# Kernel tuning notes

Measured on AMD Instinct MI355X. Metric: run time of the kernel, lower is better.

## Reference

```python
import jax, jax.numpy as jnp
import numpy as np
import math

IMG_SIZE = 768
NUM_CLASSES = 90
THRESHOLD = 0.05
IOU_THRESHOLD = 0.5
MAX_DETECTIONS = 100
K_CAND = 512  # per-class candidate pool before greedy NMS
RATIOS = [(1.0, 1.0), (1.4, 0.7), (0.7, 1.4)]
SCALES = [2 ** 0, 2 ** (1.0 / 3.0), 2 ** (2.0 / 3.0)]


def _generate_anchors():
    anchor_scale = 4.0
    pyramid_levels = [3, 4, 5, 6, 7]
    all_levels = []
    for lv in pyramid_levels:
        stride = 2 ** lv
        size = anchor_scale * 2 ** lv
        grid = IMG_SIZE // stride
        sx = np.arange(grid) * stride
        sy, sx = np.meshgrid(np.arange(grid) * stride, sx, indexing='ij')
        # torch meshgrid(shift_y, shift_x, indexing='ij') -> rows are y
        yy, xx = np.meshgrid(np.arange(grid) * stride, np.arange(grid) * stride, indexing='ij')
        shifts = np.stack([xx.ravel(), yy.ravel(), xx.ravel(), yy.ravel()], axis=1).astype(np.float32)
        base = []
        for r in RATIOS:
            for s in SCALES:
                w = size * s * math.sqrt(r[0] / r[1])
                h = size * s * math.sqrt(r[1] / r[0])
                base.append([-w / 2, -h / 2, w / 2, h / 2])
        base = np.asarray(base, dtype=np.float32)  # [9,4]
        anc = (base[None, :, :] + shifts[:, None, :]).reshape(-1, 4)
        all_levels.append(anc)
    return np.concatenate(all_levels, axis=0)  # [110484,4]


def setup_inputs() -> dict:
    key = jax.random.key(0)
    k1, k2, k3 = jax.random.split(key, 3)
    A = 110484
    x = jax.random.normal(k1, (1, 3, IMG_SIZE, IMG_SIZE), dtype=jnp.float32)
    regression = jax.random.normal(k2, (1, A, 4), dtype=jnp.float32) * 0.3
    classification = jax.random.normal(k3, (1, A, NUM_CLASSES), dtype=jnp.float32) - 2.0
    anchors = jnp.asarray(_generate_anchors())
    return {"x": x, "regression": regression, "classification": classification, "anchors": anchors}


def _decode_and_clip(anchors, deltas, H, W):
    # BBoxTransform (RetinaNet-style): deltas = (dx, dy, dw, dh)
    wa = anchors[:, 2] - anchors[:, 0]
    ha = anchors[:, 3] - anchors[:, 1]
    cxa = anchors[:, 0] + 0.5 * wa
    cya = anchors[:, 1] + 0.5 * ha
    dx, dy, dw, dh = deltas[:, 0], deltas[:, 1], deltas[:, 2], deltas[:, 3]
    cx = cxa + dx * wa
    cy = cya + dy * ha
    w = jnp.exp(dw) * wa
    h = jnp.exp(dh) * ha
    x1 = jnp.clip(cx - 0.5 * w, 0.0, W)
    y1 = jnp.clip(cy - 0.5 * h, 0.0, H)
    x2 = jnp.clip(cx + 0.5 * w, 0.0, W)
    y2 = jnp.clip(cy + 0.5 * h, 0.0, H)
    return jnp.stack([x1, y1, x2, y2], axis=1)  # [A,4]


def _pairwise_iou(b):  # [K,4] -> [K,K]
    area = (b[:, 2] - b[:, 0]) * (b[:, 3] - b[:, 1])
    xx1 = jnp.maximum(b[:, None, 0], b[None, :, 0])
    yy1 = jnp.maximum(b[:, None, 1], b[None, :, 1])
    xx2 = jnp.minimum(b[:, None, 2], b[None, :, 2])
    yy2 = jnp.minimum(b[:, None, 3], b[None, :, 3])
    inter = jnp.clip(xx2 - xx1, 0.0) * jnp.clip(yy2 - yy1, 0.0)
    return inter / (area[:, None] + area[None, :] - inter + 1e-8)


def _greedy_nms(iou_c, valid_c):
    # boxes are pre-sorted by descending score; fixed-iteration greedy NMS
    def step(suppressed, i):
        keep_i = valid_c[i] & jnp.logical_not(suppressed[i])
        suppressed = jnp.where(keep_i, suppressed | (iou_c[i] > IOU_THRESHOLD), suppressed)
        return suppressed, keep_i
    _, keep = jax.lax.scan(step, jnp.zeros(iou_c.shape[0], dtype=bool), jnp.arange(iou_c.shape[0]))
    return keep  # [K]


def _postprocess(x, regression, classification, anchors):
    H, W = x.shape[2], x.shape[3]
    boxes = _decode_and_clip(anchors, regression[0], float(H), float(W))  # [A,4]
    scores = jax.nn.sigmoid(classification[0])                            # [A,C]
    # per-class top-K candidate pool (sorted desc), fixed-shape NMS
    vals, idx = jax.lax.top_k(scores.T, K_CAND)        # [C,K]
    cand = boxes[idx]                                   # [C,K,4]
    valid = vals > THRESHOLD                            # [C,K]
    iou = jax.vmap(_pairwise_iou)(cand)                 # [C,K,K]
    keep = jax.vmap(_greedy_nms)(iou, valid)            # [C,K]
    kept_scores = jnp.where(keep, vals, -1.0).reshape(-1)  # [C*K]
    top_vals, flat_idx = jax.lax.top_k(kept_scores, MAX_DETECTIONS)
    labels = (flat_idx // K_CAND).astype(jnp.float32)
    det_boxes = cand.reshape(-1, 4)[flat_idx]
    ok = top_vals > 0.0
    det = jnp.concatenate([
        jnp.zeros((MAX_DETECTIONS, 1), dtype=jnp.float32),  # batch ids (batch=1 -> 0)
        det_boxes,
        top_vals[:, None],
        labels[:, None],
    ], axis=1)  # [100,7]
    return jnp.where(ok[:, None], det, 0.0)


def reference(x, regression, classification, anchors):
    return _postprocess(x, regression, classification, anchors)
```

## Files before the change

### kernel.cpp

```cpp
#include <hip/hip_runtime.h>
#include <math.h>


#define A_N   110484
#define C_N   90
#define KCAND 512
#define NBINS 8192
#define KSH   19
#define MAXDET 100
#define IMG_F 768.0f
#define THRESH 0.05f
#define VTOT  (A_N / 4)
#define SL_CAP 2048
#define KEEP_CAP 100
#define T_BLKS ((A_N + 63) / 64)
#define SEL_T 512
#define D_BLKS ((A_N + SEL_T - 1) / SEL_T)
#define FCAP  512

typedef unsigned int u32;
typedef unsigned long long u64;

__device__ __forceinline__ u32 fkey(float f) {
    u32 u = __float_as_uint(f);
    return (u & 0x80000000u) ? ~u : (u | 0x80000000u);
}
__device__ __forceinline__ float unfkey(u32 k) {
    u32 u = (k & 0x80000000u) ? (k ^ 0x80000000u) : ~k;
    return __uint_as_float(u);
}
__device__ __forceinline__ u64 shflx64(u64 v, int m) {
    u32 lo = (u32)__shfl_xor((int)(u32)v, m, 64);
    u32 hi = (u32)__shfl_xor((int)(v >> 32), m, 64);
    return ((u64)hi << 32) | lo;
}

__global__ __launch_bounds__(256)
void prep_kernel(const float* __restrict__ cls,
                 u32* __restrict__ keysT) {
    __shared__ u32 tile[64 * 91];
    const int a0 = blockIdx.x * 64;
    const int lim = min(64, A_N - a0);
    const int n4 = (lim * C_N) >> 2;
    const float4* src4 = (const float4*)(cls + (size_t)a0 * C_N);
    for (int i4 = threadIdx.x; i4 < n4; i4 += 256) {
        float4 x4 = src4[i4];
        const u32 base = (u32)(4 * i4);
        float xs[4] = { x4.x, x4.y, x4.z, x4.w };
        #pragma unroll
        for (int k = 0; k < 4; ++k) {
            u32 i = base + k;
            u32 aa = i / C_N, c = i % C_N;
            float s = 1.0f / (1.0f + expf(-xs[k]));
            tile[aa * 91 + c] = fkey(s);
        }
    }
    __syncthreads();
    for (int j = threadIdx.x; j < C_N * 64; j += 256) {
        int c = j >> 6, aa = j & 63;
        if (aa < lim)
            keysT[(size_t)c * A_N + a0 + aa] = tile[aa * 91 + c];
    }
}

__global__ __launch_bounds__(SEL_T)
void select_kernel(const u32* __restrict__ keysT,
                   const float* __restrict__ anchors,
                   const float* __restrict__ reg,
                   float4* __restrict__ boxes,
                   u64* __restrict__ candbuf) {
    __shared__ u32 hist[NBINS / 2];
    __shared__ u32 csum[SEL_T];
    __shared__ u64 lbuf[SL_CAP];
    __shared__ u32 sPv;
    __shared__ int lcnt;
    const int tid = threadIdx.x;

    if (blockIdx.x >= C_N) {
        int a = (blockIdx.x - C_N) * SEL_T + tid;
        if (a < A_N) {
            float4 an = ((const float4*)anchors)[a];
            float4 dl = ((const float4*)reg)[a];
            float wa = an.z - an.x, ha = an.w - an.y;
            float cx = an.x + 0.5f * wa + dl.x * wa;
            float cy = an.y + 0.5f * ha + dl.y * ha;
            float w = expf(dl.z) * wa;
            float h = expf(dl.w) * ha;
            float4 o;
            o.x = fminf(fmaxf(cx - 0.5f * w, 0.0f), IMG_F);
            o.y = fminf(fmaxf(cy - 0.5f * h, 0.0f), IMG_F);
            o.z = fminf(fmaxf(cx + 0.5f * w, 0.0f), IMG_F);
            o.w = fminf(fmaxf(cy + 0.5f * h, 0.0f), IMG_F);
            boxes[a] = o;
        }
        return;
    }
    const int c = blockIdx.x;
    const uint4* kv = (const uint4*)(keysT + (size_t)c * A_N);

    for (int i = tid; i < NBINS / 2; i += SEL_T) hist[i] = 0;
    if (tid == 0) { sPv = 0; lcnt = 0; }
    __syncthreads();

    #define HACC(K) do { \
        u32 b0 = (K).x >> KSH, b1 = (K).y >> KSH, b2 = (K).z >> KSH, b3 = (K).w >> KSH; \
        atomicAdd(&hist[b0 >> 1], 1u << ((b0 & 1) << 4)); \
        atomicAdd(&hist[b1 >> 1], 1u << ((b1 & 1) << 4)); \
        atomicAdd(&hist[b2 >> 1], 1u << ((b2 & 1) << 4)); \
        atomicAdd(&hist[b3 >> 1], 1u << ((b3 & 1) << 4)); } while (0)
    {
        int i = tid;
        for (; i + 3 * SEL_T < VTOT; i += 4 * SEL_T) {
            uint4 ka = kv[i], kb = kv[i + SEL_T], kc = kv[i + 2 * SEL_T], kd = kv[i + 3 * SEL_T];
            HACC(ka); HACC(kb); HACC(kc); HACC(kd);
        }
        for (; i < VTOT; i += SEL_T) { uint4 ka = kv[i]; HACC(ka); }
    }
    __syncthreads();

    u32 own = 0;
    {
        const int wb = (NBINS / 2) - 8 - 8 * tid;
        const int g = (tid >> 2) & 7;
        #pragma unroll
        for (int jj = 0; jj < 8; ++jj) {
            u32 v = hist[wb + ((g + jj) & 7)];
            own += (v & 0xffffu) + (v >> 16);
        }
    }
    csum[tid] = own;
    __syncthreads();
    for (int off = 1; off < SEL_T; off <<= 1) {
        u32 v = csum[tid];
        u32 a = (tid >= off) ? csum[tid - off] : 0u;
        __syncthreads();
        csum[tid] = v + a;
        __syncthreads();
    }
    const u32 incl = csum[tid], excl = incl - own;
    if (excl < (u32)KCAND && incl >= (u32)KCAND) {
        u32 cum = excl;
        const int hb = NBINS - 1 - 16 * tid;
        for (int j = 0; j < 16; ++j) {
            int b = hb - j;
            u32 v = hist[b >> 1];
            u32 cnt = (b & 1) ? (v >> 16) : (v & 0xffffu);
            if (cum + cnt >= (u32)KCAND) { sPv = (u32)b; break; }
            cum += cnt;
        }
    }
    __syncthreads();
    const u32 P = sPv;

    #define CACC(K, BASE) do { \
        if (((K).x >> KSH) >= P) { int p = atomicAdd(&lcnt, 1); if (p < SL_CAP) lbuf[p] = (((u64)(~(K).x)) << 32) | (u32)(BASE); } \
        if (((K).y >> KSH) >= P) { int p = atomicAdd(&lcnt, 1); if (p < SL_CAP) lbuf[p] = (((u64)(~(K).y)) << 32) | (u32)((BASE) + 1); } \
        if (((K).z >> KSH) >= P) { int p = atomicAdd(&lcnt, 1); if (p < SL_CAP) lbuf[p] = (((u64)(~(K).z)) << 32) | (u32)((BASE) + 2); } \
        if (((K).w >> KSH) >= P) { int p = atomicAdd(&lcnt, 1); if (p < SL_CAP) lbuf[p] = (((u64)(~(K).w)) << 32) | (u32)((BASE) + 3); } } while (0)
    {
        int i = tid;
        for (; i + 3 * SEL_T < VTOT; i += 4 * SEL_T) {
            uint4 ka = kv[i], kb = kv[i + SEL_T], kc = kv[i + 2 * SEL_T], kd = kv[i + 3 * SEL_T];
            CACC(ka, 4 * i); CACC(kb, 4 * (i + SEL_T)); CACC(kc, 4 * (i + 2 * SEL_T)); CACC(kd, 4 * (i + 3 * SEL_T));
        }
        for (; i < VTOT; i += SEL_T) { uint4 ka = kv[i]; CACC(ka, 4 * i); }
    }
    __syncthreads();
    const int n = min(lcnt, SL_CAP);
    for (int q = tid; q < SL_CAP; q += SEL_T) if (q >= n) lbuf[q] = ~0ULL;
    __syncthreads();

    {
        const int l = tid & 63, w = tid >> 6;
        int ii[4]; u64 v[4];
        #pragma unroll
        for (int r = 0; r < 4; ++r) { ii[r] = 256 * w + 64 * r + l; v[r] = lbuf[ii[r]]; }
        __syncthreads();
        #pragma unroll
        for (u32 kk = 2; kk <= (u32)SL_CAP; kk <<= 1) {
            #pragma unroll
            for (u32 j = kk >> 1; j > 0; j >>= 1) {
                if (j >= 256) {
                    #pragma unroll
                    for (int r = 0; r < 4; ++r) lbuf[ii[r]] = v[r];
                    __syncthreads();
                    #pragma unroll
                    for (int r = 0; r < 4; ++r) {
                        u64 pv = lbuf[ii[r] ^ j];
                        bool up = ((ii[r] & kk) == 0);
                        bool m = (((ii[r] & j) == 0) == up);
                        v[r] = m ? (v[r] < pv ? v[r] : pv) : (v[r] > pv ? v[r] : pv);
                    }
                    __syncthreads();
                } else if (j >= 64) {
                    const int rx = (int)(j >> 6);
                    u64 nv[4];
                    #pragma unroll
                    for (int r = 0; r < 4; ++r) {
                        u64 pv = v[r ^ rx];
                        bool up = ((ii[r] & kk) == 0);
                        bool m = (((ii[r] & j) == 0) == up);
                        nv[r] = m ? (v[r] < pv ? v[r] : pv) : (v[r] > pv ? v[r] : pv);
                    }
                    #pragma unroll
                    for (int r = 0; r < 4; ++r) v[r] = nv[r];
                } else {
                    #pragma unroll
                    for (int r = 0; r < 4; ++r) {
                        u64 pv = shflx64(v[r], (int)j);
                        bool up = ((ii[r] & kk) == 0);
                        bool m = (((ii[r] & j) == 0) == up);
                        v[r] = m ? (v[r] < pv ? v[r] : pv) : (v[r] > pv ? v[r] : pv);
                    }
                }
            }
        }
        u64* cb = candbuf + (size_t)c * KCAND;
        #pragma unroll
        for (int r = 0; r < 4; ++r)
            if (ii[r] < KCAND) cb[ii[r]] = v[r];
    }
}

__global__ __launch_bounds__(1024, 4)
void nms_kernel(const u64* __restrict__ candbuf,
                const float4* __restrict__ boxes,
                u32* __restrict__ keptbuf, u32* __restrict__ cnt2) {
    __shared__ u32 bmask[KCAND * 16];
    __shared__ float4 bb4[KCAND];
    __shared__ float sc[KCAND];
    __shared__ u32 keepf[16], wbase[17];
    const int c = blockIdx.x, tid = threadIdx.x;
    const int l = tid & 63, w = tid >> 6;

    if (tid < KCAND) {
        u64 e = candbuf[(size_t)c * KCAND + tid];
        sc[tid] = unfkey(~((u32)(e >> 32)));
        bb4[tid] = boxes[(u32)e];
    }
    if (tid < 16) keepf[tid] = 0;
    __syncthreads();

    {
        const float4 cj0 = bb4[0 * 64 + l], cj1 = bb4[1 * 64 + l];
        const float4 cj2 = bb4[2 * 64 + l], cj3 = bb4[3 * 64 + l];
        const float4 cj4 = bb4[4 * 64 + l], cj5 = bb4[5 * 64 + l];
        const float4 cj6 = bb4[6 * 64 + l], cj7 = bb4[7 * 64 + l];
        const float aj0 = (cj0.z - cj0.x) * (cj0.w - cj0.y);
        const float aj1 = (cj1.z - cj1.x) * (cj1.w - cj1.y);
        const float aj2 = (cj2.z - cj2.x) * (cj2.w - cj2.y);
        const float aj3 = (cj3.z - cj3.x) * (cj3.w - cj3.y);
        const float aj4 = (cj4.z - cj4.x) * (cj4.w - cj4.y);
        const float aj5 = (cj5.z - cj5.x) * (cj5.w - cj5.y);
        const float aj6 = (cj6.z - cj6.x) * (cj6.w - cj6.y);
        const float aj7 = (cj7.z - cj7.x) * (cj7.w - cj7.y);

        #define QSTEP(QQ, CJ, AJ) do { \
            if (QQ >= q0) { \
                float xx1 = fmaxf(bi.x, (CJ).x), yy1 = fmaxf(bi.y, (CJ).y); \
                float xx2 = fminf(bi.z, (CJ).z), yy2 = fminf(bi.w, (CJ).w); \
                float inter = fmaxf(xx2 - xx1, 0.0f) * fmaxf(yy2 - yy1, 0.0f); \
                float uni = ai + (AJ) - inter + 1e-8f; \
                bool sup = ((QQ * 64 + l) > r) && (inter > 0.5f * uni); \
                u64 bal = __ballot(sup); \
                if (l == 0) *(u64*)(row + 2 * QQ) = bal; \
            } } while (0)

        for (int r = w; r < KCAND; r += 16) {
            const float4 bi = bb4[r];
            const float ai = (bi.z - bi.x) * (bi.w - bi.y);
            const int q0 = (r + 1) >> 6;
            u32* row = bmask + r * 16;
            if (l < 2 * q0) row[l] = 0;
            QSTEP(0, cj0, aj0); QSTEP(1, cj1, aj1);
            QSTEP(2, cj2, aj2); QSTEP(3, cj3, aj3);
            QSTEP(4, cj4, aj4); QSTEP(5, cj5, aj5);
            QSTEP(6, cj6, aj6); QSTEP(7, cj7, aj7);
        }
        #undef QSTEP
    }
    __syncthreads();

    if (tid < 64) {
        const int lw = tid & 15;
        u32 removed = 0, keepw = 0;
        u32 rA[8], rB[8]; float sA[8], sB[8];
        #pragma unroll
        for (int k = 0; k < 8; ++k) { rA[k] = bmask[k * 16 + lw]; sA[k] = sc[k]; }
        #pragma unroll 1
        for (int ch = 0; ch < 64; ch += 2) {
            const int tb1 = (ch + 1) * 8;
            #pragma unroll
            for (int k = 0; k < 8; ++k) { rB[k] = bmask[(tb1 + k) * 16 + lw]; sB[k] = sc[tb1 + k]; }
            {
                const int tb = ch * 8;
                #pragma unroll
                for (int k = 0; k < 8; ++k) {
                    const int t = tb + k;
                    u32 rw = (u32)__builtin_amdgcn_readlane((int)removed, t >> 5);
                    bool d = (sA[k] > THRESH) && (((rw >> (t & 31)) & 1u) == 0u);
                    removed |= d ? rA[k] : 0u;
                    keepw |= (d && (tid == (t >> 5))) ? (1u << (t & 31)) : 0u;
                }
            }
            const int tb2 = (ch + 2 < 64) ? (ch + 2) * 8 : 0;
            #pragma unroll
            for (int k = 0; k < 8; ++k) { rA[k] = bmask[(tb2 + k) * 16 + lw]; sA[k] = sc[tb2 + k]; }
            {
                #pragma unroll
                for (int k = 0; k < 8; ++k) {
                    const int t = tb1 + k;
                    u32 rw = (u32)__builtin_amdgcn_readlane((int)removed, t >> 5);
                    bool d = (sB[k] > THRESH) && (((rw >> (t & 31)) & 1u) == 0u);
                    removed |= d ? rB[k] : 0u;
                    keepw |= (d && (tid == (t >> 5))) ? (1u << (t & 31)) : 0u;
                }
            }
            u32 cnt = (u32)__popc(keepw);
            #pragma unroll
            for (int m = 32; m; m >>= 1) cnt += (u32)__shfl_xor((int)cnt, m, 64);
            if (cnt >= (u32)KEEP_CAP) break;
        }
        if (tid < 16) keepf[tid] = keepw;
    }
    __syncthreads();

    if (tid == 0) {
        u32 t = 0;
        for (int q = 0; q < 16; ++q) { wbase[q] = t; t += __popc(keepf[q]); }
        wbase[16] = t;
        cnt2[c] = (t < (u32)KEEP_CAP) ? t : (u32)KEEP_CAP;
    }
    __syncthreads();
    if (tid < KCAND) {
        u32 word = keepf[tid >> 5];
        u32 bit = (u32)tid & 31u;
        if ((word >> bit) & 1u) {
            u32 rank = wbase[tid >> 5] + __popc(word & ((1u << bit) - 1u));
            if (rank < (u32)KEEP_CAP) {
                float s = sc[tid];
                float4 b = bb4[tid];
                uint4 a2, b2;
                a2.x = ~fkey(s);
                a2.y = (u32)(c * KCAND + tid);
                a2.z = __float_as_uint(b.x);
                a2.w = __float_as_uint(b.y);
                b2.x = __float_as_uint(b.z);
                b2.y = __float_as_uint(b.w);
                b2.z = __float_as_uint(s);
                b2.w = 0u;
                uint4* e = (uint4*)(keptbuf + ((size_t)c * KEEP_CAP + rank) * 8);
                e[0] = a2; e[1] = b2;
            }
        }
    }
}

__global__ __launch_bounds__(1024)
void final_kernel(const u32* __restrict__ keptbuf, const u32* __restrict__ cnt2,
                  float* __restrict__ out) {
    __shared__ u32 hist[NBINS];
    __shared__ u32 csum[1024];
    __shared__ u64 ebuf[FCAP];
    __shared__ u32 eidx[FCAP];
    __shared__ u32 scnt[C_N];
    __shared__ u32 sP;
    __shared__ int sN;
    const int tid = threadIdx.x;
    const int TOT = C_N * KEEP_CAP;

    for (int i = tid; i < MAXDET * 7; i += 1024) out[i] = 0.0f;
    for (int i = tid; i < NBINS; i += 1024) hist[i] = 0;
    if (tid < C_N) scnt[tid] = cnt2[tid];
    if (tid == 0) { sN = 0; sP = NBINS - 1; }
    __syncthreads();

    for (int i = tid; i < TOT; i += 1024) {
        u32 c = (u32)i / KEEP_CAP, pp = (u32)i % KEEP_CAP;
        if (pp < scnt[c]) {
            u32 khi = keptbuf[(size_t)i * 8];
            atomicAdd(&hist[khi >> KSH], 1u);
        }
    }
    __syncthreads();
    u32 own = 0; const int lo = 8 * tid;
    #pragma unroll
    for (int j = 0; j < 8; ++j) own += hist[lo + j];
    csum[tid] = own;
    __syncthreads();
    for (int off = 1; off < 1024; off <<= 1) {
        u32 v = csum[tid];
        u32 a = (tid >= off) ? csum[tid - off] : 0u;
        __syncthreads();
        csum[tid] = v + a;
        __syncthreads();
    }
    const u32 incl = csum[tid], excl = incl - own;
    if (excl < (u32)MAXDET && incl >= (u32)MAXDET) {
        u32 cum = excl;
        for (int j = 0; j < 8; ++j) {
            u32 h = hist[lo + j];
            if (cum + h >= (u32)MAXDET) { sP = (u32)(lo + j); break; }
            cum += h;
        }
    }
    __syncthreads();
    const u32 P = sP;
    for (int i = tid; i < TOT; i += 1024) {
        u32 c = (u32)i / KEEP_CAP, pp = (u32)i % KEEP_CAP;
        if (pp < scnt[c]) {
            const uint2 v2 = *((const uint2*)(keptbuf + (size_t)i * 8));
            if ((v2.x >> KSH) <= P) {
                int p = atomicAdd(&sN, 1);
                if (p < FCAP) {
                    ebuf[p] = ((u64)v2.x << 32) | v2.y;
                    eidx[p] = (u32)i;
                }
            }
        }
    }
    __syncthreads();
    const int n = min(sN, FCAP);
    u32 m = 128; while ((int)m < n) m <<= 1;
    for (int i = tid; i < (int)m; i += 1024) if (i >= n) ebuf[i] = ~0ULL;
    __syncthreads();
    for (u32 kk = 2; kk <= m; kk <<= 1) {
        for (u32 j = kk >> 1; j > 0; j >>= 1) {
            u32 i = (u32)tid;
            if (i < m) {
                u32 ixj = i ^ j;
                if (ixj > i) {
                    u64 x = ebuf[i], y = ebuf[ixj];
                    bool up = ((i & kk) == 0);
                    if (up ? (x > y) : (x < y)) {
                        ebuf[i] = y; ebuf[ixj] = x;
                        u32 t = eidx[i]; eidx[i] = eidx[ixj]; eidx[ixj] = t;
                    }
                }
            }
            __syncthreads();
        }
    }
    if (tid < MAXDET && tid < n) {
        u64 comp = ebuf[tid];
        if (comp != ~0ULL) {
            const uint4* e = (const uint4*)(keptbuf + (size_t)eidx[tid] * 8);
            uint4 a = e[0], b = e[1];
            float* o = out + tid * 7;
            o[0] = 0.0f;
            o[1] = __uint_as_float(a.z); o[2] = __uint_as_float(a.w);
            o[3] = __uint_as_float(b.x); o[4] = __uint_as_float(b.y);
            o[5] = __uint_as_float(b.z);
            o[6] = (float)(((u32)comp) >> 9);
        }
    }
}

extern "C" void kernel_launch(void* const* d_in, const int* in_sizes, int n_in,
                              void* d_out, int out_size, void* d_ws, size_t ws_size,
                              hipStream_t stream) {
    const float* reg     = (const float*)d_in[1];
    const float* cls     = (const float*)d_in[2];
    const float* anchors = (const float*)d_in[3];
    float* out = (float*)d_out;

    char* ws = (char*)d_ws;
    size_t off = 0;
    auto alloc = [&](size_t bytes) -> void* {
        void* p = ws + off;
        off = (off + bytes + 255) & ~(size_t)255;
        return p;
    };
    u32*    keysT   = (u32*)   alloc((size_t)C_N * A_N * sizeof(u32));
    float4* boxes   = (float4*)alloc((size_t)A_N * sizeof(float4));
    u64*    candbuf = (u64*)   alloc((size_t)C_N * KCAND * sizeof(u64));
    u32*    keptbuf = (u32*)   alloc((size_t)C_N * KEEP_CAP * 8 * sizeof(u32));
    u32*    cnt2    = (u32*)   alloc((size_t)C_N * sizeof(u32));
    (void)ws_size;

    prep_kernel<<<T_BLKS, 256, 0, stream>>>(cls, keysT);
    select_kernel<<<C_N + D_BLKS, SEL_T, 0, stream>>>(keysT, anchors, reg, boxes, candbuf);
    nms_kernel<<<C_N, 1024, 0, stream>>>(candbuf, boxes, keptbuf, cnt2);
    final_kernel<<<1, 1024, 0, stream>>>(keptbuf, cnt2, out);
}
```

Baseline: 204.0 us.

## Move box decoding into prep kernel and double select block size

Box decoding moves from extra blocks of the select kernel into extra blocks of the prep kernel, so the select kernel launches only the 90 per-class blocks. The select kernel now uses 1024 threads per block, with deeper 8-way unrolled key loads and a rebalanced histogram scan and bitonic sort that holds two elements per thread. The aim is more parallelism and memory-level parallelism per class, since only 90 blocks run on a GPU with many CUs. The trade-off is more register and LDS pressure per block and more block-wide barriers in the scan.

Result: faster. 190.1 us (-6.8%).

```diff
diff --git a/kernel.cpp b/kernel.cpp
--- a/kernel.cpp
+++ b/kernel.cpp
@@ -14,8 +14,8 @@
 #define SL_CAP 2048
 #define KEEP_CAP 100
 #define T_BLKS ((A_N + 63) / 64)
-#define SEL_T 512
-#define D_BLKS ((A_N + SEL_T - 1) / SEL_T)
+#define PD_BLKS ((A_N + 255) / 256)
+#define SEL_T 1024
 #define FCAP  512
 
 typedef unsigned int u32;
@@ -37,8 +37,30 @@
 
 __global__ __launch_bounds__(256)
 void prep_kernel(const float* __restrict__ cls,
-                 u32* __restrict__ keysT) {
+                 const float* __restrict__ anchors,
+                 const float* __restrict__ reg,
+                 u32* __restrict__ keysT,
+                 float4* __restrict__ boxes) {
     __shared__ u32 tile[64 * 91];
+    if (blockIdx.x >= T_BLKS) {
+        int a = (blockIdx.x - T_BLKS) * 256 + threadIdx.x;
+        if (a < A_N) {
+            float4 an = ((const float4*)anchors)[a];
+            float4 dl = ((const float4*)reg)[a];
+            float wa = an.z - an.x, ha = an.w - an.y;
+            float cx = an.x + 0.5f * wa + dl.x * wa;
+            float cy = an.y + 0.5f * ha + dl.y * ha;
+            float w = expf(dl.z) * wa;
+            float h = expf(dl.w) * ha;
+            float4 o;
+            o.x = fminf(fmaxf(cx - 0.5f * w, 0.0f), IMG_F);
+            o.y = fminf(fmaxf(cy - 0.5f * h, 0.0f), IMG_F);
+            o.z = fminf(fmaxf(cx + 0.5f * w, 0.0f), IMG_F);
+            o.w = fminf(fmaxf(cy + 0.5f * h, 0.0f), IMG_F);
+            boxes[a] = o;
+        }
+        return;
+    }
     const int a0 = blockIdx.x * 64;
     const int lim = min(64, A_N - a0);
     const int n4 = (lim * C_N) >> 2;
@@ -65,9 +87,6 @@
 
 __global__ __launch_bounds__(SEL_T)
 void select_kernel(const u32* __restrict__ keysT,
-                   const float* __restrict__ anchors,
-                   const float* __restrict__ reg,
-                   float4* __restrict__ boxes,
                    u64* __restrict__ candbuf) {
     __shared__ u32 hist[NBINS / 2];
     __shared__ u32 csum[SEL_T];
@@ -75,26 +94,6 @@
     __shared__ u32 sPv;
     __shared__ int lcnt;
     const int tid = threadIdx.x;
-
-    if (blockIdx.x >= C_N) {
-        int a = (blockIdx.x - C_N) * SEL_T + tid;
-        if (a < A_N) {
-            float4 an = ((const float4*)anchors)[a];
-            float4 dl = ((const float4*)reg)[a];
-            float wa = an.z - an.x, ha = an.w - an.y;
-            float cx = an.x + 0.5f * wa + dl.x * wa;
-            float cy = an.y + 0.5f * ha + dl.y * ha;
-            float w = expf(dl.z) * wa;
-            float h = expf(dl.w) * ha;
-            float4 o;
-            o.x = fminf(fmaxf(cx - 0.5f * w, 0.0f), IMG_F);
-            o.y = fminf(fmaxf(cy - 0.5f * h, 0.0f), IMG_F);
-            o.z = fminf(fmaxf(cx + 0.5f * w, 0.0f), IMG_F);
-            o.w = fminf(fmaxf(cy + 0.5f * h, 0.0f), IMG_F);
-            boxes[a] = o;
-        }
-        return;
-    }
     const int c = blockIdx.x;
     const uint4* kv = (const uint4*)(keysT + (size_t)c * A_N);
 
@@ -110,9 +109,11 @@
         atomicAdd(&hist[b3 >> 1], 1u << ((b3 & 1) << 4)); } while (0)
     {
         int i = tid;
-        for (; i + 3 * SEL_T < VTOT; i += 4 * SEL_T) {
-            uint4 ka = kv[i], kb = kv[i + SEL_T], kc = kv[i + 2 * SEL_T], kd = kv[i + 3 * SEL_T];
-            HACC(ka); HACC(kb); HACC(kc); HACC(kd);
+        for (; i + 7 * SEL_T < VTOT; i += 8 * SEL_T) {
+            uint4 k0 = kv[i], k1 = kv[i + SEL_T], k2 = kv[i + 2 * SEL_T], k3 = kv[i + 3 * SEL_T];
+            uint4 k4 = kv[i + 4 * SEL_T], k5 = kv[i + 5 * SEL_T], k6 = kv[i + 6 * SEL_T], k7 = kv[i + 7 * SEL_T];
+            HACC(k0); HACC(k1); HACC(k2); HACC(k3);
+            HACC(k4); HACC(k5); HACC(k6); HACC(k7);
         }
         for (; i < VTOT; i += SEL_T) { uint4 ka = kv[i]; HACC(ka); }
     }
@@ -120,11 +121,11 @@
 
     u32 own = 0;
     {
-        const int wb = (NBINS / 2) - 8 - 8 * tid;
-        const int g = (tid >> 2) & 7;
+        const int wb = (NBINS / 2) - 4 - 4 * tid;
+        const int g = (tid >> 3) & 3;
         #pragma unroll
-        for (int jj = 0; jj < 8; ++jj) {
-            u32 v = hist[wb + ((g + jj) & 7)];
+        for (int jj = 0; jj < 4; ++jj) {
+            u32 v = hist[wb + ((g + jj) & 3)];
             own += (v & 0xffffu) + (v >> 16);
         }
     }
@@ -140,8 +141,8 @@
     const u32 incl = csum[tid], excl = incl - own;
     if (excl < (u32)KCAND && incl >= (u32)KCAND) {
         u32 cum = excl;
-        const int hb = NBINS - 1 - 16 * tid;
-        for (int j = 0; j < 16; ++j) {
+        const int hb = NBINS - 1 - 8 * tid;
+        for (int j = 0; j < 8; ++j) {
             int b = hb - j;
             u32 v = hist[b >> 1];
             u32 cnt = (b & 1) ? (v >> 16) : (v & 0xffffu);
@@ -159,9 +160,11 @@
         if (((K).w >> KSH) >= P) { int p = atomicAdd(&lcnt, 1); if (p < SL_CAP) lbuf[p] = (((u64)(~(K).w)) << 32) | (u32)((BASE) + 3); } } while (0)
     {
         int i = tid;
-        for (; i + 3 * SEL_T < VTOT; i += 4 * SEL_T) {
-            uint4 ka = kv[i], kb = kv[i + SEL_T], kc = kv[i + 2 * SEL_T], kd = kv[i + 3 * SEL_T];
-            CACC(ka, 4 * i); CACC(kb, 4 * (i + SEL_T)); CACC(kc, 4 * (i + 2 * SEL_T)); CACC(kd, 4 * (i + 3 * SEL_T));
+        for (; i + 7 * SEL_T < VTOT; i += 8 * SEL_T) {
+            uint4 k0 = kv[i], k1 = kv[i + SEL_T], k2 = kv[i + 2 * SEL_T], k3 = kv[i + 3 * SEL_T];
+            uint4 k4 = kv[i + 4 * SEL_T], k5 = kv[i + 5 * SEL_T], k6 = kv[i + 6 * SEL_T], k7 = kv[i + 7 * SEL_T];
+            CACC(k0, 4 * i); CACC(k1, 4 * (i + SEL_T)); CACC(k2, 4 * (i + 2 * SEL_T)); CACC(k3, 4 * (i + 3 * SEL_T));
+            CACC(k4, 4 * (i + 4 * SEL_T)); CACC(k5, 4 * (i + 5 * SEL_T)); CACC(k6, 4 * (i + 6 * SEL_T)); CACC(k7, 4 * (i + 7 * SEL_T));
         }
         for (; i < VTOT; i += SEL_T) { uint4 ka = kv[i]; CACC(ka, 4 * i); }
     }
@@ -172,53 +175,39 @@
 
     {
         const int l = tid & 63, w = tid >> 6;
-        int ii[4]; u64 v[4];
-        #pragma unroll
-        for (int r = 0; r < 4; ++r) { ii[r] = 256 * w + 64 * r + l; v[r] = lbuf[ii[r]]; }
+        const int i0 = 128 * w + l, i1 = i0 + 64;
+        u64 v0 = lbuf[i0], v1 = lbuf[i1];
         __syncthreads();
         #pragma unroll
         for (u32 kk = 2; kk <= (u32)SL_CAP; kk <<= 1) {
             #pragma unroll
             for (u32 j = kk >> 1; j > 0; j >>= 1) {
-                if (j >= 256) {
-                    #pragma unroll
-                    for (int r = 0; r < 4; ++r) lbuf[ii[r]] = v[r];
+                if (j >= 128) {
+                    lbuf[i0] = v0; lbuf[i1] = v1;
                     __syncthreads();
-                    #pragma unroll
-                    for (int r = 0; r < 4; ++r) {
-                        u64 pv = lbuf[ii[r] ^ j];
-                        bool up = ((ii[r] & kk) == 0);
-                        bool m = (((ii[r] & j) == 0) == up);
-                        v[r] = m ? (v[r] < pv ? v[r] : pv) : (v[r] > pv ? v[r] : pv);
-                    }
+                    u64 w0 = lbuf[i0 ^ j], w1 = lbuf[i1 ^ j];
+                    bool m0 = (((i0 & j) == 0) == ((i0 & kk) == 0));
+                    bool m1 = (((i1 & j) == 0) == ((i1 & kk) == 0));
+                    v0 = m0 ? (v0 < w0 ? v0 : w0) : (v0 > w0 ? v0 : w0);
+                    v1 = m1 ? (v1 < w1 ? v1 : w1) : (v1 > w1 ? v1 : w1);
                     __syncthreads();
-                } else if (j >= 64) {
-                    const int rx = (int)(j >> 6);
-                    u64 nv[4];
-                    #pragma unroll
-                    for (int r = 0; r < 4; ++r) {
-                        u64 pv = v[r ^ rx];
-                        bool up = ((ii[r] & kk) == 0);
-                        bool m = (((ii[r] & j) == 0) == up);
-                        nv[r] = m ? (v[r] < pv ? v[r] : pv) : (v[r] > pv ? v[r] : pv);
-                    }
-                    #pragma unroll
-                    for (int r = 0; r < 4; ++r) v[r] = nv[r];
+                } else if (j == 64) {
+                    bool up = ((i0 & kk) == 0);
+                    u64 mn = v0 < v1 ? v0 : v1, mx = v0 < v1 ? v1 : v0;
+                    v0 = up ? mn : mx; v1 = up ? mx : mn;
                 } else {
-                    #pragma unroll
-                    for (int r = 0; r < 4; ++r) {
-                        u64 pv = shflx64(v[r], (int)j);
-                        bool up = ((ii[r] & kk) == 0);
-                        bool m = (((ii[r] & j) == 0) == up);
-                        v[r] = m ? (v[r] < pv ? v[r] : pv) : (v[r] > pv ? v[r] : pv);
-                    }
+                    u64 w0 = shflx64(v0, (int)j), w1 = shflx64(v1, (int)j);
+                    bool m0 = (((i0 & j) == 0) == ((i0 & kk) == 0));
+                    bool m1 = (((i1 & j) == 0) == ((i1 & kk) == 0));
+                    v0 = m0 ? (v0 < w0 ? v0 : w0) : (v0 > w0 ? v0 : w0);
+                    v1 = m1 ? (v1 < w1 ? v1 : w1) : (v1 > w1 ? v1 : w1);
                 }
             }
         }
-        u64* cb = candbuf + (size_t)c * KCAND;
-        #pragma unroll
-        for (int r = 0; r < 4; ++r)
-            if (ii[r] < KCAND) cb[ii[r]] = v[r];
+        if (w < 4) {
+            u64* cb = candbuf + (size_t)c * KCAND;
+            cb[i0] = v0; cb[i1] = v1;
+        }
     }
 }
 
@@ -478,8 +467,8 @@
     u32*    cnt2    = (u32*)   alloc((size_t)C_N * sizeof(u32));
     (void)ws_size;
 
-    prep_kernel<<<T_BLKS, 256, 0, stream>>>(cls, keysT);
-    select_kernel<<<C_N + D_BLKS, SEL_T, 0, stream>>>(keysT, anchors, reg, boxes, candbuf);
+    prep_kernel<<<T_BLKS + PD_BLKS, 256, 0, stream>>>(cls, anchors, reg, keysT, boxes);
+    select_kernel<<<C_N, SEL_T, 0, stream>>>(keysT, candbuf);
     nms_kernel<<<C_N, 1024, 0, stream>>>(candbuf, boxes, keptbuf, cnt2);
     final_kernel<<<1, 1024, 0, stream>>>(keptbuf, cnt2, out);
 }
```
